# Performance work log

Hardware: AMD Instinct MI355X
Metric: run time of the kernel (lower is better)

Reference implementation:

```python
import jax, jax.numpy as jnp
import numpy as np

D_MODEL = 1024
NUM_HEADS = 16
D_K = D_MODEL // NUM_HEADS  # 64
THETA = 10000.0
BATCH = 2
SEQ = 2048


def _init_linear(key, out_f, in_f):
    std = np.sqrt(2.0 / (in_f + out_f))
    w = jax.random.truncated_normal(key, -3.0, 3.0, (out_f, in_f), dtype=jnp.float32)
    return w * std


def setup_inputs() -> dict:
    key = jax.random.key(0)
    kx, kq, kk, kv, ko = jax.random.split(key, 5)
    x = jax.random.normal(kx, (BATCH, SEQ, D_MODEL), dtype=jnp.float32)
    token_positions = jnp.arange(SEQ, dtype=jnp.int64 if jax.config.jax_enable_x64 else jnp.int32)
    Wq = _init_linear(kq, D_MODEL, D_MODEL)
    Wk = _init_linear(kk, D_MODEL, D_MODEL)
    Wv = _init_linear(kv, D_MODEL, D_MODEL)
    Wo = _init_linear(ko, D_MODEL, D_MODEL)
    return {"x": x, "token_positions": token_positions,
            "Wq": Wq, "Wk": Wk, "Wv": Wv, "Wo": Wo}


def _rope(x, token_positions):
    # x: (b, h, s, d_k). Interleaved-pair rotation, matching the torch module:
    # even' = even*cos - odd*sin ; odd' = even*sin + odd*cos
    d_half = D_K // 2
    pos = token_positions.astype(jnp.float32)[:, None]          # (s, 1)
    dims = jnp.arange(d_half, dtype=jnp.float32)[None, :]       # (1, d_half)
    angles = pos / (THETA ** (2.0 * dims / D_K))                 # (s, d_half)
    cos, sin = jnp.cos(angles), jnp.sin(angles)                  # (s, d_half)
    even = x[..., 0::2]                                          # (b,h,s,d_half)
    odd = x[..., 1::2]
    r_even = even * cos - odd * sin
    r_odd = even * sin + odd * cos
    # re-interleave pairs -> (b,h,s,d_k)
    out = jnp.stack([r_even, r_odd], axis=-1)
    return out.reshape(*x.shape[:-1], D_K)


def reference(x, token_positions, Wq, Wk, Wv, Wo):
    b, s, _ = x.shape
    # Linear: x @ W.T
    def proj(W):
        y = jnp.einsum('bsd,ed->bse', x, W)
        return y.reshape(b, s, NUM_HEADS, D_K).transpose(0, 2, 1, 3)  # (b,h,s,dk)
    Q, K, V = proj(Wq), proj(Wk), proj(Wv)
    Q = _rope(Q, token_positions)
    K = _rope(K, token_positions)
    scale = 1.0 / np.sqrt(D_K)
    scores = jnp.einsum('bhqd,bhkd->bhqk', Q, K) * scale           # (b,h,s,s)
    causal = jnp.tril(jnp.ones((s, s), dtype=bool))
    scores = jnp.where(causal, scores, -jnp.inf)
    weights = jax.nn.softmax(scores, axis=-1)
    attn = jnp.einsum('bhqk,bhkd->bhqd', weights, V)
    attn = attn.transpose(0, 2, 1, 3).reshape(b, s, NUM_HEADS * D_K)
    return jnp.einsum('bse,de->bsd', attn, Wo)
```

## Files before the change

### kernel.cpp

```cpp
#include <hip/hip_runtime.h>
#include <hip/hip_bf16.h>
#include <math.h>

typedef __attribute__((ext_vector_type(4))) float   f32x4;
typedef __attribute__((ext_vector_type(8))) __bf16  bf16x8;
typedef __attribute__((ext_vector_type(8))) unsigned short ushort8;
typedef unsigned short u16;

#define QSCALE 0.1803368801111729f

__device__ __forceinline__ u16 f2b(float f) {
    unsigned u = __builtin_bit_cast(unsigned, f);
    u += 0x7fff + ((u >> 16) & 1);
    return (u16)(u >> 16);
}
__device__ __forceinline__ void gl16(const void* g, void* l) {
    __builtin_amdgcn_global_load_lds((const __attribute__((address_space(1))) void*)g,
                                     (__attribute__((address_space(3))) void*)l, 16, 0, 0);
}
__device__ __forceinline__ int pos32(int d) {
    return ((d & 15) >> 2) * 8 + ((d >> 4) & 1) * 4 + (d & 3);
}
__device__ __forceinline__ bf16x8 frag128(const u16* tile, int row, int half, int lg) {
    int gran = (half * 4 + lg) ^ (row & 7);
    return *(const bf16x8*)(tile + row * 64 + gran * 8);
}

__device__ __forceinline__ int permq(int i) {
    int q = i & 7;
    return (i & ~7) | ((q & 3) * 2 + (q >> 2));
}
__global__ void prep_kernel(const float* __restrict__ x,
                            const float* __restrict__ Wq, const float* __restrict__ Wk,
                            const float* __restrict__ Wv, const float* __restrict__ Wo,
                            const int* __restrict__ pos,
                            u16* __restrict__ xb, u16* __restrict__ wqkv, u16* __restrict__ wob,
                            float2* __restrict__ csn)
{
    int bx = blockIdx.x, tid = threadIdx.x;
    if (bx < 4096) {
        int i = bx * 256 + tid;
        float4 v = ((const float4*)x)[i];
        ((ushort4*)xb)[permq(i)] = make_ushort4(f2b(v.x), f2b(v.y), f2b(v.z), f2b(v.w));
    } else if (bx < 8192) {
        int j = bx - 4096;
        int w = j >> 10;
        int i = (j & 1023) * 256 + tid;
        const float* s = (w == 0) ? Wq : (w == 1) ? Wk : (w == 2) ? Wv : Wo;
        u16* d = (w == 3) ? wob : (wqkv + (size_t)w * 1048576);
        float4 v = ((const float4*)s)[i];
        ((ushort4*)d)[permq(i)] = make_ushort4(f2b(v.x), f2b(v.y), f2b(v.z), f2b(v.w));
    } else {
        int idx = (bx - 8192) * 256 + tid;
        int s = idx >> 5, i = idx & 31;
        float p = (float)pos[s];
        float ang = p * exp2f((float)i * (-13.28771237954945f / 32.f));
        csn[idx] = make_float2(cosf(ang), sinf(ang));
    }
}

#define GEMM_STAGE(A_, B_, Kd_, kt_, dA_, dB_)                                              \
    _Pragma("unroll")                                                                       \
    for (int r = 0; r < 4; ++r) {                                                           \
        int c = r * 256 + tid;                                                              \
        int row = c >> 3;                                                                   \
        int col = (((c & 7) ^ (row & 7))) * 8;                                              \
        gl16((A_) + (size_t)(mblk + row) * (Kd_) + (kt_) + col, (dA_) + c * 8);             \
        gl16((B_) + (size_t)(nblk + row) * (Kd_) + (kt_) + col, (dB_) + c * 8);             \
    }

#define GEMM_CORE(A_, B_, Kd_)                                                              \
    GEMM_STAGE(A_, B_, Kd_, 0, lsA, lsB)                                                    \
    for (int it = 0; it < (Kd_) >> 6; ++it) {                                               \
        const int cur = it & 1;                                                             \
        const u16* cA = lsA + cur * 8192;                                                   \
        const u16* cB = lsB + cur * 8192;                                                   \
        __syncthreads();                \
        if (it + 1 < ((Kd_) >> 6)) {                                                        \
            GEMM_STAGE(A_, B_, Kd_, (it + 1) * 64, lsA + (cur ^ 1) * 8192,                  \
                       lsB + (cur ^ 1) * 8192)                                              \
        }                                                                                   \
        bf16x8 af[4][2], bfr[4][2];                                                         \
        _Pragma("unroll")                                                                   \
        for (int mm = 0; mm < 4; ++mm) {                                                    \
            af[mm][0] = frag128(cA, m0 + mm * 16 + l15, 0, lg);                             \
            af[mm][1] = frag128(cA, m0 + mm * 16 + l15, 1, lg);                             \
        }                                                                                   \
        _Pragma("unroll")                                                                   \
        for (int nn = 0; nn < 4; ++nn) {                                                    \
            bfr[nn][0] = frag128(cB, n0 + nn * 16 + l15, 0, lg);                            \
            bfr[nn][1] = frag128(cB, n0 + nn * 16 + l15, 1, lg);                            \
        }                                                                                   \
        _Pragma("unroll")                                                                   \
        for (int mm = 0; mm < 4; ++mm)                                                      \
            _Pragma("unroll")                                                               \
            for (int nn = 0; nn < 4; ++nn) {                                                \
                acc[mm][nn] = __builtin_amdgcn_mfma_f32_16x16x32_bf16(af[mm][0], bfr[nn][0], acc[mm][nn], 0, 0, 0); \
                acc[mm][nn] = __builtin_amdgcn_mfma_f32_16x16x32_bf16(af[mm][1], bfr[nn][1], acc[mm][nn], 0, 0, 0); \
            }                                                                               \
    }

__global__ __launch_bounds__(256) void gemm_qkv(
    const u16* __restrict__ A, const u16* __restrict__ Bw, const float2* __restrict__ csn,
    u16* __restrict__ Qh, u16* __restrict__ Kh, u16* __restrict__ Vt)
{
    __shared__ u16 shm[32768];
    u16* lsA = shm;
    u16* lsB = shm + 16384;
    const int tid = threadIdx.x;
    const int lane = tid & 63, wv = tid >> 6;
    const int l15 = lane & 15, lg = lane >> 4;
    const int id = blockIdx.x;
    const int xcd = id & 7, slot = id >> 3;
    const int bx = (xcd & 1) * 12 + slot % 12;
    const int by = (xcd >> 1) * 8 + slot / 12;
    const int mblk = by * 128, nblk = bx * 128;
    const int m0 = (wv >> 1) * 64, n0 = (wv & 1) * 64;

    f32x4 acc[4][4];
    for (int a = 0; a < 4; ++a)
        for (int b = 0; b < 4; ++b)
            for (int r = 0; r < 4; ++r) acc[a][b][r] = 0.f;

    GEMM_CORE(A, Bw, 1024)

    const int role = nblk >> 10;
    if (role < 2) {
        u16* dst = role ? Kh : Qh;
        const float scale = role ? 1.f : QSCALE;
#pragma unroll
        for (int mm = 0; mm < 4; ++mm)
#pragma unroll
            for (int nn = 0; nn < 4; ++nn) {
                int colq = (nblk + n0 + nn * 16 + l15) & 1023;
                int h = colq >> 6, dd = colq & 63;
                int outd = (dd & 32) + pos32(dd & 31);
                int odd = dd & 1, i = dd >> 1;
#pragma unroll
                for (int r = 0; r < 4; ++r) {
                    int rowg = mblk + m0 + mm * 16 + lg * 4 + r;
                    int b = rowg >> 11, s = rowg & 2047;
                    float2 cs = csn[s * 32 + i];
                    float v = acc[mm][nn][r];
                    float p = __shfl_xor(v, 1);
                    float o = odd ? (p * cs.y + v * cs.x) : (v * cs.x - p * cs.y);
                    dst[((size_t)(b * 16 + h) * 2048 + s) * 64 + outd] = f2b(o * scale);
                }
            }
    } else {
        __syncthreads();
#pragma unroll
        for (int mm = 0; mm < 4; ++mm)
#pragma unroll
            for (int nn = 0; nn < 4; ++nn)
#pragma unroll
                for (int r = 0; r < 4; ++r)
                    shm[(m0 + mm * 16 + lg * 4 + r) * 132 + n0 + nn * 16 + l15] = f2b(acc[mm][nn][r]);
        __syncthreads();
        const int el = tid >> 1, half = tid & 1;
        const int colg = nblk - 2048 + el;
        const int h = colg >> 6, dd = colg & 63;
        const int b = mblk >> 11;
        const int sbase = (mblk & 2047) + half * 64;
        u16 vals[64];
#pragma unroll
        for (int o = 0; o < 64; ++o) {
            int oo = o & 31;
            int d = (o & 32) + ((oo >> 2) & 1) * 16 + (oo >> 3) * 4 + (oo & 3);
            vals[o] = shm[(half * 64 + d) * 132 + el];
        }
        u16* dst = Vt + ((size_t)(b * 16 + h) * 64 + dd) * 2048 + sbase;
#pragma unroll
        for (int a = 0; a < 8; ++a)
            *(ushort8*)(dst + a * 8) = *(const ushort8*)(vals + a * 8);
    }
}

__global__ __launch_bounds__(256) void gemm_bt(
    const u16* __restrict__ A, const u16* __restrict__ Bw, float* __restrict__ Cf)
{
    __shared__ u16 shm[32768];
    u16* lsA = shm;
    u16* lsB = shm + 16384;
    const int tid = threadIdx.x;
    const int lane = tid & 63, wv = tid >> 6;
    const int l15 = lane & 15, lg = lane >> 4;
    const int id = blockIdx.x;
    const int xcd = id & 7, slot = id >> 3;
    const int bx = (xcd & 1) * 4 + (slot & 3);
    const int by = (xcd >> 1) * 8 + (slot >> 2);
    const int mblk = by * 128, nblk = bx * 128;
    const int m0 = (wv >> 1) * 64, n0 = (wv & 1) * 64;

    f32x4 acc[4][4];
    for (int a = 0; a < 4; ++a)
        for (int b = 0; b < 4; ++b)
            for (int r = 0; r < 4; ++r) acc[a][b][r] = 0.f;

    GEMM_CORE(A, Bw, 1024)

#pragma unroll
    for (int mm = 0; mm < 4; ++mm)
#pragma unroll
        for (int nn = 0; nn < 4; ++nn)
#pragma unroll
            for (int r = 0; r < 4; ++r) {
                int row = mblk + m0 + mm * 16 + lg * 4 + r;
                int col = nblk + n0 + nn * 16 + l15;
                Cf[(size_t)row * 1024 + col] = acc[mm][nn][r];
            }
}

__device__ __forceinline__ void stage_kv128(const u16* Kp, const u16* Vp, int t,
                                            u16* bK, u16* bV, int tid, int wv) {
#pragma unroll
    for (int r = 0; r < 2; ++r) {
        int c = r * 512 + tid;
        int krow = c >> 3;
        int kcol = ((c & 7) ^ (krow & 7)) * 8;
        gl16(Kp + (size_t)(t * 128 + krow) * 64 + kcol, bK + (r * 512 + wv * 64) * 8);
        int d = krow & 63, ss = krow >> 6;
        int vcol = ((c & 7) ^ (d & 7)) * 8;
        gl16(Vp + (size_t)d * 2048 + t * 128 + ss * 64 + vcol, bV + (r * 512 + wv * 64) * 8);
    }
}
__global__ __launch_bounds__(512) void attn_kernel(
    const u16* __restrict__ Qh, const u16* __restrict__ Kh, const u16* __restrict__ Vt,
    u16* __restrict__ Oa)
{
    __shared__ u16 shm[32768];
    const int tid = threadIdx.x;
    const int lane = tid & 63, wv = tid >> 6;
    const int l15 = lane & 15, lg = lane >> 4;
    const int id = blockIdx.x;
    const int gq = id >> 5;
    const int qt = (id < 256) ? (15 - gq) : (gq - 8);
    const int bh = id & 31;
    const int b = bh >> 4, h = bh & 15;
    const u16* Qp = Qh + (size_t)bh * 2048 * 64;
    const u16* Kp = Kh + (size_t)bh * 2048 * 64;
    const u16* Vp = Vt + (size_t)bh * 64 * 2048;

#pragma unroll
    for (int r = 0; r < 2; ++r) {
        int c = r * 512 + tid;
        int row = c >> 3;
        int col = ((c & 7) ^ (row & 7)) * 8;
        gl16(Qp + (size_t)(qt * 128 + row) * 64 + col, shm + (r * 512 + wv * 64) * 8);
    }
    __syncthreads();
    bf16x8 qf[2];
#pragma unroll
    for (int ds = 0; ds < 2; ++ds)
        qf[ds] = frag128(shm, wv * 16 + l15, ds, lg);
    __syncthreads();

    stage_kv128(Kp, Vp, 0, shm, shm + 16384, tid, wv);
    __syncthreads();

    f32x4 accO[4];
#pragma unroll
    for (int dm = 0; dm < 4; ++dm)
        for (int r = 0; r < 4; ++r) accO[dm][r] = 0.f;
    float mrun = -3e38f, lrun = 0.f;
    const int st_b = 2 * qt + (wv >> 2);
    const int NT = qt + 1;

    for (int t = 0; t < NT; ++t) {
        const int cur = t & 1;
        if (t + 1 < NT)
            stage_kv128(Kp, Vp, t + 1, shm + (cur ^ 1) * 8192, shm + 16384 + (cur ^ 1) * 8192, tid, wv);
        const u16* Kt = shm + cur * 8192;
        const u16* Vb = shm + 16384 + cur * 8192;
#pragma unroll
        for (int ss = 0; ss < 2; ++ss) {
            const int st = 2 * t + ss;
            if (st <= st_b) {
                f32x4 sa[4];
                __builtin_amdgcn_s_setprio(1);
#pragma unroll
                for (int kb = 0; kb < 4; ++kb) {
                    int krow = ss * 64 + kb * 16 + l15;
                    bf16x8 kf0 = frag128(Kt, krow, 0, lg);
                    bf16x8 kf1 = frag128(Kt, krow, 1, lg);
                    f32x4 s = { 0.f, 0.f, 0.f, 0.f };
                    s = __builtin_amdgcn_mfma_f32_16x16x32_bf16(kf0, qf[0], s, 0, 0, 0);
                    s = __builtin_amdgcn_mfma_f32_16x16x32_bf16(kf1, qf[1], s, 0, 0, 0);
                    sa[kb] = s;
                }
                __builtin_amdgcn_s_setprio(0);
                if (st == st_b) {
                    int qg = qt * 128 + wv * 16 + l15;
#pragma unroll
                    for (int kb = 0; kb < 4; ++kb)
#pragma unroll
                        for (int r = 0; r < 4; ++r)
                            if (st * 64 + kb * 16 + lg * 4 + r > qg) sa[kb][r] = -1e30f;
                }
                float a0 = fmaxf(fmaxf(sa[0][0], sa[0][1]), fmaxf(sa[0][2], sa[0][3]));
                float a1 = fmaxf(fmaxf(sa[1][0], sa[1][1]), fmaxf(sa[1][2], sa[1][3]));
                float a2 = fmaxf(fmaxf(sa[2][0], sa[2][1]), fmaxf(sa[2][2], sa[2][3]));
                float a3 = fmaxf(fmaxf(sa[3][0], sa[3][1]), fmaxf(sa[3][2], sa[3][3]));
                float pm = fmaxf(fmaxf(a0, a1), fmaxf(a2, a3));
                pm = fmaxf(pm, __shfl_xor(pm, 16));
                pm = fmaxf(pm, __shfl_xor(pm, 32));
                if (!__all(pm <= mrun + 8.f)) {
                    float mnew = fmaxf(mrun, pm);
                    float fac = exp2f(mrun - mnew);
                    lrun *= fac;
#pragma unroll
                    for (int dm = 0; dm < 4; ++dm)
#pragma unroll
                        for (int r = 0; r < 4; ++r) accO[dm][r] *= fac;
                    mrun = mnew;
                }
                float ps = 0.f;
#pragma unroll
                for (int kb = 0; kb < 4; ++kb)
#pragma unroll
                    for (int r = 0; r < 4; ++r) {
                        float pe = exp2f(sa[kb][r] - mrun);
                        sa[kb][r] = pe;
                        ps += pe;
                    }
                ps += __shfl_xor(ps, 16);
                ps += __shfl_xor(ps, 32);
                lrun += ps;
                bf16x8 pf[2];
#pragma unroll
                for (int ks = 0; ks < 2; ++ks) {
                    bf16x8 tt;
#pragma unroll
                    for (int j = 0; j < 4; ++j) {
                        tt[j]     = (__bf16)sa[2 * ks][j];
                        tt[4 + j] = (__bf16)sa[2 * ks + 1][j];
                    }
                    pf[ks] = tt;
                }
                __builtin_amdgcn_s_setprio(1);
#pragma unroll
                for (int dm = 0; dm < 4; ++dm) {
                    int vrow = ss * 64 + dm * 16 + l15;
#pragma unroll
                    for (int ks = 0; ks < 2; ++ks) {
                        bf16x8 vf = frag128(Vb, vrow, ks, lg);
                        accO[dm] = __builtin_amdgcn_mfma_f32_16x16x32_bf16(vf, pf[ks], accO[dm], 0, 0, 0);
                    }
                }
                __builtin_amdgcn_s_setprio(0);
            }
        }
        __syncthreads();
    }
    float inv = 1.f / lrun;
    int srow = qt * 128 + wv * 16 + l15;
#pragma unroll
    for (int dm = 0; dm < 4; ++dm) {
        int cb = h * 64 + dm * 16 + lg * 4;
        int q = (cb >> 2) & 7;
        int cbp = (cb & ~31) | (((q & 3) * 2 + (q >> 2)) * 4);
        ushort4 o = make_ushort4(f2b(accO[dm][0] * inv), f2b(accO[dm][1] * inv),
                                 f2b(accO[dm][2] * inv), f2b(accO[dm][3] * inv));
        *(ushort4*)&Oa[((size_t)b * 2048 + srow) * 1024 + cbp] = o;
    }
}

extern "C" void kernel_launch(void* const* d_in, const int* in_sizes, int n_in,
                              void* d_out, int out_size, void* d_ws, size_t ws_size,
                              hipStream_t stream) {
    const float* x  = (const float*)d_in[0];
    const int*   pos = (const int*)d_in[1];
    const float* Wq = (const float*)d_in[2];
    const float* Wk = (const float*)d_in[3];
    const float* Wv = (const float*)d_in[4];
    const float* Wo = (const float*)d_in[5];
    float* out = (float*)d_out;
    char* ws = (char*)d_ws;
    const size_t MB = 1024 * 1024;
    u16*    xb   = (u16*)   (ws + 0);
    u16*    wqkv = (u16*)   (ws + 8  * MB);
    u16*    wob  = (u16*)   (ws + 14 * MB);
    float2* csn  = (float2*)(ws + 16 * MB);
    u16*    Qh   = (u16*)   (ws + 24 * MB);
    u16*    Kh   = (u16*)   (ws + 32 * MB);
    u16*    Vt   = (u16*)   (ws + 40 * MB);
    u16*    Oa   = (u16*)   (ws + 48 * MB);

    prep_kernel<<<8448, 256, 0, stream>>>(x, Wq, Wk, Wv, Wo, pos, xb, wqkv, wob, csn);

    gemm_qkv<<<768, 256, 0, stream>>>(xb, wqkv, csn, Qh, Kh, Vt);

    attn_kernel<<<512, 512, 0, stream>>>(Qh, Kh, Vt, Oa);

    gemm_bt<<<256, 256, 0, stream>>>(Oa, wob, out);
}
```

Before: 109.6 us.

## Split attention KV range across two blocks and merge partial softmax results

Each query tile's causal KV range is now split into two halves processed by separate blocks (1024 blocks instead of 512), each writing unnormalized bf16 partial outputs plus running max and sum. A new merge kernel combines the two partials with rescaling and writes the interleaved output layout. KV staging drops from 128-row to 64-row tiles, halving shared memory. The aim is better load balance and occupancy across CUs, at the cost of an extra launch, extra global traffic, and bf16 rounding of the partials.

```diff
diff --git a/kernel.cpp b/kernel.cpp
--- a/kernel.cpp
+++ b/kernel.cpp
@@ -13,6 +13,10 @@
     unsigned u = __builtin_bit_cast(unsigned, f);
     u += 0x7fff + ((u >> 16) & 1);
     return (u16)(u >> 16);
+}
+__device__ __forceinline__ float b2f(u16 h) {
+    unsigned u = ((unsigned)h) << 16;
+    return __builtin_bit_cast(float, u);
 }
 __device__ __forceinline__ void gl16(const void* g, void* l) {
     __builtin_amdgcn_global_load_lds((const __attribute__((address_space(1))) void*)g,
@@ -211,35 +215,31 @@
             }
 }
 
-__device__ __forceinline__ void stage_kv128(const u16* Kp, const u16* Vp, int t,
-                                            u16* bK, u16* bV, int tid, int wv) {
-#pragma unroll
-    for (int r = 0; r < 2; ++r) {
-        int c = r * 512 + tid;
-        int krow = c >> 3;
-        int kcol = ((c & 7) ^ (krow & 7)) * 8;
-        gl16(Kp + (size_t)(t * 128 + krow) * 64 + kcol, bK + (r * 512 + wv * 64) * 8);
-        int d = krow & 63, ss = krow >> 6;
-        int vcol = ((c & 7) ^ (d & 7)) * 8;
-        gl16(Vp + (size_t)d * 2048 + t * 128 + ss * 64 + vcol, bV + (r * 512 + wv * 64) * 8);
-    }
+__device__ __forceinline__ void stage_kv64(const u16* Kp, const u16* Vp, int st,
+                                           u16* bK, u16* bV, int tid) {
+    int row = tid >> 3;
+    int col = ((tid & 7) ^ (row & 7)) * 8;
+    gl16(Kp + (size_t)(st * 64 + row) * 64 + col, bK + tid * 8);
+    gl16(Vp + (size_t)row * 2048 + st * 64 + col, bV + tid * 8);
 }
 __global__ __launch_bounds__(512) void attn_kernel(
     const u16* __restrict__ Qh, const u16* __restrict__ Kh, const u16* __restrict__ Vt,
-    u16* __restrict__ Oa)
+    u16* __restrict__ Op, float2* __restrict__ Oml)
 {
-    __shared__ u16 shm[32768];
+    __shared__ u16 shm[16384];
     const int tid = threadIdx.x;
     const int lane = tid & 63, wv = tid >> 6;
     const int l15 = lane & 15, lg = lane >> 4;
-    const int id = blockIdx.x;
-    const int gq = id >> 5;
-    const int qt = (id < 256) ? (15 - gq) : (gq - 8);
-    const int bh = id & 31;
-    const int b = bh >> 4, h = bh & 15;
+    const int u = blockIdx.x;
+    const int inner = u & 511, half = u >> 9;
+    const int gq = inner >> 5;
+    const int qt = (inner < 256) ? (15 - gq) : (gq - 8);
+    const int bh = inner & 31;
     const u16* Qp = Qh + (size_t)bh * 2048 * 64;
     const u16* Kp = Kh + (size_t)bh * 2048 * 64;
     const u16* Vp = Vt + (size_t)bh * 64 * 2048;
+    const int lo = half ? (qt + 1) : 0;
+    const int hi = half ? (2 * qt + 2) : (qt + 1);
 
 #pragma unroll
     for (int r = 0; r < 2; ++r) {
@@ -255,7 +255,7 @@
         qf[ds] = frag128(shm, wv * 16 + l15, ds, lg);
     __syncthreads();
 
-    stage_kv128(Kp, Vp, 0, shm, shm + 16384, tid, wv);
+    stage_kv64(Kp, Vp, lo, shm, shm + 8192, tid);
     __syncthreads();
 
     f32x4 accO[4];
@@ -264,104 +264,132 @@
         for (int r = 0; r < 4; ++r) accO[dm][r] = 0.f;
     float mrun = -3e38f, lrun = 0.f;
     const int st_b = 2 * qt + (wv >> 2);
-    const int NT = qt + 1;
-
-    for (int t = 0; t < NT; ++t) {
-        const int cur = t & 1;
-        if (t + 1 < NT)
-            stage_kv128(Kp, Vp, t + 1, shm + (cur ^ 1) * 8192, shm + 16384 + (cur ^ 1) * 8192, tid, wv);
-        const u16* Kt = shm + cur * 8192;
-        const u16* Vb = shm + 16384 + cur * 8192;
-#pragma unroll
-        for (int ss = 0; ss < 2; ++ss) {
-            const int st = 2 * t + ss;
-            if (st <= st_b) {
-                f32x4 sa[4];
-                __builtin_amdgcn_s_setprio(1);
-#pragma unroll
-                for (int kb = 0; kb < 4; ++kb) {
-                    int krow = ss * 64 + kb * 16 + l15;
-                    bf16x8 kf0 = frag128(Kt, krow, 0, lg);
-                    bf16x8 kf1 = frag128(Kt, krow, 1, lg);
-                    f32x4 s = { 0.f, 0.f, 0.f, 0.f };
-                    s = __builtin_amdgcn_mfma_f32_16x16x32_bf16(kf0, qf[0], s, 0, 0, 0);
-                    s = __builtin_amdgcn_mfma_f32_16x16x32_bf16(kf1, qf[1], s, 0, 0, 0);
-                    sa[kb] = s;
+
+    for (int st = lo; st < hi; ++st) {
+        const int cur = (st - lo) & 1;
+        if (st + 1 < hi)
+            stage_kv64(Kp, Vp, st + 1, shm + (cur ^ 1) * 4096, shm + 8192 + (cur ^ 1) * 4096, tid);
+        const u16* Kt = shm + cur * 4096;
+        const u16* Vb = shm + 8192 + cur * 4096;
+        if (st <= st_b) {
+            f32x4 sa[4];
+            __builtin_amdgcn_s_setprio(1);
+#pragma unroll
+            for (int kb = 0; kb < 4; ++kb) {
+                int krow = kb * 16 + l15;
+                bf16x8 kf0 = frag128(Kt, krow, 0, lg);
+                bf16x8 kf1 = frag128(Kt, krow, 1, lg);
+                f32x4 s = { 0.f, 0.f, 0.f, 0.f };
+                s = __builtin_amdgcn_mfma_f32_16x16x32_bf16(kf0, qf[0], s, 0, 0, 0);
+                s = __builtin_amdgcn_mfma_f32_16x16x32_bf16(kf1, qf[1], s, 0, 0, 0);
+                sa[kb] = s;
+            }
+            __builtin_amdgcn_s_setprio(0);
+            if (st == st_b) {
+                int qg = qt * 128 + wv * 16 + l15;
+#pragma unroll
+                for (int kb = 0; kb < 4; ++kb)
+#pragma unroll
+                    for (int r = 0; r < 4; ++r)
+                        if (st * 64 + kb * 16 + lg * 4 + r > qg) sa[kb][r] = -1e30f;
+            }
+            float a0 = fmaxf(fmaxf(sa[0][0], sa[0][1]), fmaxf(sa[0][2], sa[0][3]));
+            float a1 = fmaxf(fmaxf(sa[1][0], sa[1][1]), fmaxf(sa[1][2], sa[1][3]));
+            float a2 = fmaxf(fmaxf(sa[2][0], sa[2][1]), fmaxf(sa[2][2], sa[2][3]));
+            float a3 = fmaxf(fmaxf(sa[3][0], sa[3][1]), fmaxf(sa[3][2], sa[3][3]));
+            float pm = fmaxf(fmaxf(a0, a1), fmaxf(a2, a3));
+            pm = fmaxf(pm, __shfl_xor(pm, 16));
+            pm = fmaxf(pm, __shfl_xor(pm, 32));
+            if (!__all(pm <= mrun + 8.f)) {
+                float mnew = fmaxf(mrun, pm);
+                float fac = exp2f(mrun - mnew);
+                lrun *= fac;
+#pragma unroll
+                for (int dm = 0; dm < 4; ++dm)
+#pragma unroll
+                    for (int r = 0; r < 4; ++r) accO[dm][r] *= fac;
+                mrun = mnew;
+            }
+            float ps = 0.f;
+#pragma unroll
+            for (int kb = 0; kb < 4; ++kb)
+#pragma unroll
+                for (int r = 0; r < 4; ++r) {
+                    float pe = exp2f(sa[kb][r] - mrun);
+                    sa[kb][r] = pe;
+                    ps += pe;
                 }
-                __builtin_amdgcn_s_setprio(0);
-                if (st == st_b) {
-                    int qg = qt * 128 + wv * 16 + l15;
-#pragma unroll
-                    for (int kb = 0; kb < 4; ++kb)
-#pragma unroll
-                        for (int r = 0; r < 4; ++r)
-                            if (st * 64 + kb * 16 + lg * 4 + r > qg) sa[kb][r] = -1e30f;
+            ps += __shfl_xor(ps, 16);
+            ps += __shfl_xor(ps, 32);
+            lrun += ps;
+            bf16x8 pf[2];
+#pragma unroll
+            for (int ks = 0; ks < 2; ++ks) {
+                bf16x8 tt;
+#pragma unroll
+                for (int j = 0; j < 4; ++j) {
+                    tt[j]     = (__bf16)sa[2 * ks][j];
+                    tt[4 + j] = (__bf16)sa[2 * ks + 1][j];
                 }
-                float a0 = fmaxf(fmaxf(sa[0][0], sa[0][1]), fmaxf(sa[0][2], sa[0][3]));
-                float a1 = fmaxf(fmaxf(sa[1][0], sa[1][1]), fmaxf(sa[1][2], sa[1][3]));
-                float a2 = fmaxf(fmaxf(sa[2][0], sa[2][1]), fmaxf(sa[2][2], sa[2][3]));
-                float a3 = fmaxf(fmaxf(sa[3][0], sa[3][1]), fmaxf(sa[3][2], sa[3][3]));
-                float pm = fmaxf(fmaxf(a0, a1), fmaxf(a2, a3));
-                pm = fmaxf(pm, __shfl_xor(pm, 16));
-                pm = fmaxf(pm, __shfl_xor(pm, 32));
-                if (!__all(pm <= mrun + 8.f)) {
-                    float mnew = fmaxf(mrun, pm);
-                    float fac = exp2f(mrun - mnew);
-                    lrun *= fac;
-#pragma unroll
-                    for (int dm = 0; dm < 4; ++dm)
-#pragma unroll
-                        for (int r = 0; r < 4; ++r) accO[dm][r] *= fac;
-                    mrun = mnew;
+                pf[ks] = tt;
+            }
+            __builtin_amdgcn_s_setprio(1);
+#pragma unroll
+            for (int dm = 0; dm < 4; ++dm) {
+                int vrow = dm * 16 + l15;
+#pragma unroll
+                for (int ks = 0; ks < 2; ++ks) {
+                    bf16x8 vf = frag128(Vb, vrow, ks, lg);
+                    accO[dm] = __builtin_amdgcn_mfma_f32_16x16x32_bf16(vf, pf[ks], accO[dm], 0, 0, 0);
                 }
-                float ps = 0.f;
-#pragma unroll
-                for (int kb = 0; kb < 4; ++kb)
-#pragma unroll
-                    for (int r = 0; r < 4; ++r) {
-                        float pe = exp2f(sa[kb][r] - mrun);
-                        sa[kb][r] = pe;
-                        ps += pe;
-                    }
-                ps += __shfl_xor(ps, 16);
-                ps += __shfl_xor(ps, 32);
-                lrun += ps;
-                bf16x8 pf[2];
-#pragma unroll
-                for (int ks = 0; ks < 2; ++ks) {
-                    bf16x8 tt;
-#pragma unroll
-                    for (int j = 0; j < 4; ++j) {
-                        tt[j]     = (__bf16)sa[2 * ks][j];
-                        tt[4 + j] = (__bf16)sa[2 * ks + 1][j];
-                    }
-                    pf[ks] = tt;
-                }
-                __builtin_amdgcn_s_setprio(1);
-#pragma unroll
-                for (int dm = 0; dm < 4; ++dm) {
-                    int vrow = ss * 64 + dm * 16 + l15;
-#pragma unroll
-                    for (int ks = 0; ks < 2; ++ks) {
-                        bf16x8 vf = frag128(Vb, vrow, ks, lg);
-                        accO[dm] = __builtin_amdgcn_mfma_f32_16x16x32_bf16(vf, pf[ks], accO[dm], 0, 0, 0);
-                    }
-                }
-                __builtin_amdgcn_s_setprio(0);
-            }
+            }
+            __builtin_amdgcn_s_setprio(0);
         }
         __syncthreads();
     }
-    float inv = 1.f / lrun;
-    int srow = qt * 128 + wv * 16 + l15;
+    const int qloc = wv * 16 + l15;
+    u16* op = Op + ((size_t)u * 128 + qloc) * 64;
 #pragma unroll
     for (int dm = 0; dm < 4; ++dm) {
-        int cb = h * 64 + dm * 16 + lg * 4;
+        ushort4 o = make_ushort4(f2b(accO[dm][0]), f2b(accO[dm][1]),
+                                 f2b(accO[dm][2]), f2b(accO[dm][3]));
+        *(ushort4*)(op + dm * 16 + lg * 4) = o;
+    }
+    if (lg == 0) Oml[u * 128 + qloc] = make_float2(mrun, lrun);
+}
+
+__global__ __launch_bounds__(256) void attn_merge(
+    const u16* __restrict__ Op, const float2* __restrict__ Oml, u16* __restrict__ Oa)
+{
+    const int inner = blockIdx.x;
+    const int gq = inner >> 5;
+    const int qt = (inner < 256) ? (15 - gq) : (gq - 8);
+    const int bh = inner & 31;
+    const int b = bh >> 4, h = bh & 15;
+    const int t = threadIdx.x;
+    const int row = t >> 1, dh = (t & 1) * 32;
+    float2 ml1 = Oml[inner * 128 + row];
+    float2 ml2 = Oml[(inner + 512) * 128 + row];
+    float m = fmaxf(ml1.x, ml2.x);
+    float f1 = exp2f(ml1.x - m), f2 = exp2f(ml2.x - m);
+    float inv = 1.f / (f1 * ml1.y + f2 * ml2.y);
+    float s1 = f1 * inv, s2 = f2 * inv;
+    const u16* p1 = Op + ((size_t)inner * 128 + row) * 64 + dh;
+    const u16* p2 = Op + ((size_t)(inner + 512) * 128 + row) * 64 + dh;
+    const int srow = qt * 128 + row;
+    u16* dst = Oa + ((size_t)b * 2048 + srow) * 1024 + h * 64;
+#pragma unroll
+    for (int a = 0; a < 8; ++a) {
+        ushort4 a1 = *(const ushort4*)(p1 + a * 4);
+        ushort4 a2 = *(const ushort4*)(p2 + a * 4);
+        int cb = dh + a * 4;
         int q = (cb >> 2) & 7;
         int cbp = (cb & ~31) | (((q & 3) * 2 + (q >> 2)) * 4);
-        ushort4 o = make_ushort4(f2b(accO[dm][0] * inv), f2b(accO[dm][1] * inv),
-                                 f2b(accO[dm][2] * inv), f2b(accO[dm][3] * inv));
-        *(ushort4*)&Oa[((size_t)b * 2048 + srow) * 1024 + cbp] = o;
+        ushort4 o = make_ushort4(f2b(s1 * b2f(a1.x) + s2 * b2f(a2.x)),
+                                 f2b(s1 * b2f(a1.y) + s2 * b2f(a2.y)),
+                                 f2b(s1 * b2f(a1.z) + s2 * b2f(a2.z)),
+                                 f2b(s1 * b2f(a1.w) + s2 * b2f(a2.w)));
+        *(ushort4*)(dst + cbp) = o;
     }
 }
 
@@ -379,18 +407,21 @@
     const size_t MB = 1024 * 1024;
     u16*    xb   = (u16*)   (ws + 0);
     u16*    wqkv = (u16*)   (ws + 8  * MB);
-    u16*    wob  = (u16*)   (ws + 14 * MB);
     float2* csn  = (float2*)(ws + 16 * MB);
+    u16*    wob  = (u16*)   (ws + 17 * MB);
+    float2* Oml  = (float2*)(ws + 19 * MB);
     u16*    Qh   = (u16*)   (ws + 24 * MB);
     u16*    Kh   = (u16*)   (ws + 32 * MB);
     u16*    Vt   = (u16*)   (ws + 40 * MB);
     u16*    Oa   = (u16*)   (ws + 48 * MB);
+    u16*    Op   = (u16*)   (ws + 0);
 
     prep_kernel<<<8448, 256, 0, stream>>>(x, Wq, Wk, Wv, Wo, pos, xb, wqkv, wob, csn);
 
     gemm_qkv<<<768, 256, 0, stream>>>(xb, wqkv, csn, Qh, Kh, Vt);
 
-    attn_kernel<<<512, 512, 0, stream>>>(Qh, Kh, Vt, Oa);
+    attn_kernel<<<1024, 512, 0, stream>>>(Qh, Kh, Vt, Op, Oml);
+    attn_merge<<<512, 256, 0, stream>>>(Op, Oml, Oa);
 
     gemm_bt<<<256, 256, 0, stream>>>(Oa, wob, out);
 }
```

After: 115.9 us. +5.7%, slower.
